# Kernel tuning notes

Measured on AMD Instinct MI355X. Metric: run time of the kernel, lower is better.

Reference implementation:

```python
import jax, jax.numpy as jnp
import numpy as np
from functools import partial

BATCH, SEQ = 2, 2048
D_MODEL, D_INNER, D_XB = 2048, 4096, 1024
HEADDIM, D_STATE = 64, 64
NHEADS = D_INNER // HEADDIM      # 64
NKV = D_XB // HEADDIM            # 16
REP = NHEADS // NKV              # 4
INTER = 8192
EPS = 1e-5
D_IN_PROJ = D_INNER + D_XB + D_XB + D_INNER + NHEADS  # z, x, B, C, dt


def setup_inputs() -> dict:
    key = jax.random.key(0)
    ks = jax.random.split(key, 8)
    g = lambda k, shape, s: (jax.random.normal(k, shape, jnp.float32) * s)
    return {
        "hidden_states": g(ks[0], (BATCH, SEQ, D_MODEL), 1.0),
        "ln_w": jnp.ones((D_MODEL,), jnp.float32),
        "ln_b": jnp.zeros((D_MODEL,), jnp.float32),
        "in_proj_w": g(ks[1], (D_IN_PROJ, D_MODEL), 0.02),
        "dt_bias": jax.random.uniform(ks[2], (NHEADS,), jnp.float32, -4.0, 0.0),
        "A_log": jnp.log(jnp.arange(1, NHEADS + 1, dtype=jnp.float32)),
        "Dp": jnp.ones((NHEADS,), jnp.float32),
        "norm_w": jnp.ones((D_INNER,), jnp.float32),
        "out_proj_w": g(ks[3], (D_MODEL, D_INNER), 0.02),
        "fc1_w": g(ks[4], (INTER, D_MODEL), 0.02),
        "fc1_b": jnp.zeros((INTER,), jnp.float32),
        "fc2_w": g(ks[5], (D_MODEL, INTER), 0.02),
        "fc2_b": jnp.zeros((D_MODEL,), jnp.float32),
    }


def _layernorm(x, w, b):
    mu = x.mean(-1, keepdims=True)
    var = ((x - mu) ** 2).mean(-1, keepdims=True)
    return (x - mu) * jax.lax.rsqrt(var + EPS) * w + b


def _ssd_scan(xh, dt, A, Bh, Ch):
    # xh: (b,l,h,p)  dt: (b,l,h)  A: (h,)  Bh,Ch: (b,l,h,n)
    dA = jnp.exp(dt * A)  # (b,l,h) discrete decay
    to_l = lambda t: jnp.moveaxis(t, 1, 0)  # time-major for scan

    def step(state, inp):
        dA_t, dt_t, x_t, B_t, C_t = inp
        state = state * dA_t[:, :, None, None] + jnp.einsum(
            "bh,bhp,bhn->bhpn", dt_t, x_t, B_t)
        y = jnp.einsum("bhpn,bhn->bhp", state, C_t)
        return state, y

    state0 = jnp.zeros((xh.shape[0], NHEADS, HEADDIM, D_STATE), xh.dtype)
    _, ys = jax.lax.scan(step, state0, (to_l(dA), to_l(dt), to_l(xh), to_l(Bh), to_l(Ch)))
    return jnp.moveaxis(ys, 0, 1)  # (b,l,h,p)


def reference(hidden_states, ln_w, ln_b, in_proj_w, dt_bias, A_log, Dp,
              norm_w, out_proj_w, fc1_w, fc1_b, fc2_w, fc2_b):
    residual = hidden_states
    h = _layernorm(hidden_states, ln_w, ln_b)

    # ---- Mamba2 branch ----
    zxbcdt = h @ in_proj_w.T  # (b,l,D_IN_PROJ)
    z, x, Bm, Cm, dt = jnp.split(
        zxbcdt, np.cumsum([D_INNER, D_XB, D_XB, D_INNER]).tolist(), axis=-1)
    b, l = h.shape[0], h.shape[1]
    dt = jax.nn.softplus(dt + dt_bias)               # (b,l,nheads)
    A = -jnp.exp(A_log)                              # (nheads,)
    # GQA-style repeat of x (values) and B (keys) from NKV to NHEADS groups
    xh = jnp.repeat(x.reshape(b, l, NKV, HEADDIM), REP, axis=2)   # (b,l,h,p)
    Bh = jnp.repeat(Bm.reshape(b, l, NKV, D_STATE), REP, axis=2)  # (b,l,h,n)
    Ch = Cm.reshape(b, l, NHEADS, D_STATE)                        # (b,l,h,n)

    y = _ssd_scan(xh, dt, A, Bh, Ch) + Dp[None, None, :, None] * xh
    yf = y.reshape(b, l, D_INNER)
    # gated RMSNorm (norm_before_gate=False): gate first, then rmsnorm
    yf = yf * jax.nn.silu(z)
    yf = yf * jax.lax.rsqrt((yf * yf).mean(-1, keepdims=True) + EPS) * norm_w
    mamba_out = yf @ out_proj_w.T

    # ---- Phi MLP branch (parallel, shares the layernormed input) ----
    mlp = jax.nn.gelu(h @ fc1_w.T + fc1_b, approximate=True) @ fc2_w.T + fc2_b

    # resid_dropout is identity in eval mode
    return mamba_out + mlp + residual
```

## Files before the change

### kernel.cpp

```cpp
#include <hip/hip_runtime.h>
#include <hip/hip_bf16.h>

#define BATCH 2
#define SEQ   2048
#define DMODEL 2048
#define DINNER 4096
#define DXB   1024
#define NHEADS 64
#define NKV   16
#define HEADDIM 64
#define DSTATE 64
#define INTER 8192
#define DINPROJ 10304
#define ROWS  (BATCH*SEQ)
#define NC    32
#define EPSV  1e-5f

typedef short short8 __attribute__((ext_vector_type(8)));
typedef float f32x4 __attribute__((ext_vector_type(4)));

typedef const __attribute__((address_space(1))) unsigned int cg_u32;
typedef __attribute__((address_space(3))) unsigned int ls_u32;

static __device__ __forceinline__ void gll16(const void* g, void* l) {
    __builtin_amdgcn_global_load_lds((cg_u32*)g, (ls_u32*)l, 16, 0, 0);
}

static __device__ __forceinline__ unsigned short f2bf(float f) {
    unsigned int u = __float_as_uint(f);
    unsigned int r = (u + 0x7fffu + ((u >> 16) & 1u)) >> 16;
    return (unsigned short)r;
}
static __device__ __forceinline__ float bf2f(unsigned short h) {
    return __uint_as_float(((unsigned int)h) << 16);
}

__global__ __launch_bounds__(256) void convk(const float* __restrict__ in,
                                             unsigned short* __restrict__ out, int n4) {
    int stride = gridDim.x * blockDim.x;
    for (int i = blockIdx.x * blockDim.x + threadIdx.x; i < n4; i += stride) {
        float4 v = ((const float4*)in)[i];
        ushort4 o;
        o.x = f2bf(v.x); o.y = f2bf(v.y); o.z = f2bf(v.z); o.w = f2bf(v.w);
        ((ushort4*)out)[i] = o;
    }
}

__global__ __launch_bounds__(256) void ln_kernel(const float* __restrict__ x,
                                                 const float* __restrict__ w,
                                                 const float* __restrict__ b,
                                                 unsigned short* __restrict__ hout) {
    int row = blockIdx.x;
    int t = threadIdx.x;
    const float* xr = x + (size_t)row * DMODEL;
    float v[8];
    float4 v0 = *(const float4*)&xr[t * 8];
    float4 v1 = *(const float4*)&xr[t * 8 + 4];
    v[0]=v0.x; v[1]=v0.y; v[2]=v0.z; v[3]=v0.w; v[4]=v1.x; v[5]=v1.y; v[6]=v1.z; v[7]=v1.w;
    float s = 0.f, s2 = 0.f;
    #pragma unroll
    for (int i = 0; i < 8; ++i) { s += v[i]; s2 += v[i]*v[i]; }
    #pragma unroll
    for (int off = 1; off < 64; off <<= 1) { s += __shfl_xor(s, off); s2 += __shfl_xor(s2, off); }
    __shared__ float sa[4], sb[4];
    int lane = t & 63, wv = t >> 6;
    if (lane == 0) { sa[wv] = s; sb[wv] = s2; }
    __syncthreads();
    s = sa[0]+sa[1]+sa[2]+sa[3];
    s2 = sb[0]+sb[1]+sb[2]+sb[3];
    float mu = s / DMODEL;
    float var = s2 / DMODEL - mu * mu;
    float sc = rsqrtf(var + EPSV);
    unsigned short* ho = hout + (size_t)row * DMODEL + t * 8;
    #pragma unroll
    for (int i = 0; i < 8; ++i) {
        int d = t * 8 + i;
        ho[i] = f2bf((v[i] - mu) * sc * w[d] + b[d]);
    }
}

#define SLOTSZ 49152
template <int EPI>
__global__ __launch_bounds__(512, 2) void gemm_p(
    const unsigned short* __restrict__ A, const unsigned short* __restrict__ B,
    int M, int N, int K, int nby,
    float* __restrict__ outF, unsigned short* __restrict__ outH,
    const float* __restrict__ bias, const float* __restrict__ add1,
    const float* __restrict__ add2) {
    __shared__ __align__(16) char smem[3 * SLOTSZ];
    int t = threadIdx.x, lane = t & 63, w = t >> 6;
    int nwg = gridDim.x, cpx = nwg >> 3;
    int logical = (blockIdx.x & 7) * cpx + (blockIdx.x >> 3);
    int by = logical % nby, bx = logical / nby;
    int brow = by * 128, bcol = bx * 256;
    int wr = w >> 2, wc = w & 3;
    int wrb = wr * 64, wcb = wc * 64;

    int lr8 = lane >> 3;
    int lch = ((lane & 7) ^ lr8) << 3;
    const unsigned short* pa[2];
    #pragma unroll
    for (int j = 0; j < 2; ++j)
        pa[j] = A + (size_t)(brow + w * 16 + j * 8 + lr8) * K + lch;
    const unsigned short* pb[4];
    #pragma unroll
    for (int j = 0; j < 4; ++j) {
        int r = bcol + w * 32 + j * 8 + lr8;
        if (r > N - 1) r = N - 1;
        pb[j] = B + (size_t)r * K + lch;
    }
    auto stageA = [&](int slot, int j) {
        gll16(pa[j], smem + slot * SLOTSZ + (w * 16 + j * 8) * 128);
        pa[j] += 64;
    };
    auto stageB = [&](int slot, int j) {
        gll16(pb[j], smem + slot * SLOTSZ + 16384 + (w * 32 + j * 8) * 128);
        pb[j] += 64;
    };

    int arow = lane & 15;
    int swz0 = (((lane >> 4) ^ (lane & 7)) << 4);

    f32x4 acc[4][4] = {};
    const int NT = K >> 6;
    #pragma unroll
    for (int j = 0; j < 2; ++j) stageA(0, j);
    #pragma unroll
    for (int j = 0; j < 4; ++j) stageB(0, j);
    #pragma unroll
    for (int j = 0; j < 2; ++j) stageA(1, j);
    #pragma unroll
    for (int j = 0; j < 4; ++j) stageB(1, j);

    int slot = 0, slot2 = 2;
    for (int kt = 0; kt < NT; ++kt) {
        if (kt + 1 < NT) { asm volatile("s_waitcnt vmcnt(6)" ::: "memory"); }
        else             { asm volatile("s_waitcnt vmcnt(0)" ::: "memory"); }
        __builtin_amdgcn_s_barrier();
        asm volatile("" ::: "memory");
        const char* Ab = smem + slot * SLOTSZ;
        const char* Bb = Ab + 16384;
        bool st = (kt + 2 < NT);
        short8 af[4], bfv[4];
        #pragma unroll
        for (int f = 0; f < 4; ++f)
            af[f] = *(const short8*)(Ab + (wrb + f * 16 + arow) * 128 + swz0);
        #pragma unroll
        for (int n = 0; n < 4; ++n)
            bfv[n] = *(const short8*)(Bb + (wcb + n * 16 + arow) * 128 + swz0);
        if (st) { stageA(slot2, 0); stageA(slot2, 1); stageB(slot2, 0); }
        __builtin_amdgcn_s_setprio(1);
        #pragma unroll
        for (int f = 0; f < 4; ++f)
            #pragma unroll
            for (int n = 0; n < 4; ++n)
                acc[f][n] = __builtin_amdgcn_mfma_f32_16x16x32_bf16(af[f], bfv[n], acc[f][n], 0, 0, 0);
        __builtin_amdgcn_s_setprio(0);
        #pragma unroll
        for (int f = 0; f < 4; ++f)
            af[f] = *(const short8*)(Ab + (wrb + f * 16 + arow) * 128 + (swz0 ^ 64));
        #pragma unroll
        for (int n = 0; n < 4; ++n)
            bfv[n] = *(const short8*)(Bb + (wcb + n * 16 + arow) * 128 + (swz0 ^ 64));
        if (st) { stageB(slot2, 1); stageB(slot2, 2); stageB(slot2, 3); }
        __builtin_amdgcn_s_setprio(1);
        #pragma unroll
        for (int f = 0; f < 4; ++f)
            #pragma unroll
            for (int n = 0; n < 4; ++n)
                acc[f][n] = __builtin_amdgcn_mfma_f32_16x16x32_bf16(af[f], bfv[n], acc[f][n], 0, 0, 0);
        __builtin_amdgcn_s_setprio(0);
        slot  = (slot  == 2) ? 0 : slot + 1;
        slot2 = (slot2 == 2) ? 0 : slot2 + 1;
    }

    int rlane = (lane >> 4) << 2, clane = lane & 15;
    #pragma unroll
    for (int f = 0; f < 4; ++f) {
        #pragma unroll
        for (int n = 0; n < 4; ++n) {
            int col = bcol + wcb + n * 16 + clane;
            if (col < N) {
                #pragma unroll
                for (int j = 0; j < 4; ++j) {
                    int row = brow + wrb + f * 16 + rlane + j;
                    size_t idx = (size_t)row * N + col;
                    float v = acc[f][n][j];
                    if constexpr (EPI == 0) {
                        outF[idx] = v;
                    } else if constexpr (EPI == 1) {
                        v += bias[col];
                        float g = 0.5f * v * (1.f + tanhf(0.7978845608f * (v + 0.044715f * v * v * v)));
                        outH[idx] = f2bf(g);
                    } else if constexpr (EPI == 2) {
                        outF[idx] = v + bias[col] + add1[idx] + add2[idx];
                    } else {
                        outH[idx] = f2bf(v);
                    }
                }
            }
        }
    }
}

__global__ __launch_bounds__(256) void dtk(const unsigned short* __restrict__ zx,
                                           const float* __restrict__ dt_bias,
                                           const float* __restrict__ A_log,
                                           float* __restrict__ dtv, float* __restrict__ dtA) {
    int idx = blockIdx.x * 256 + threadIdx.x;
    int h = idx & 63;
    size_t row = idx >> 6;
    float raw = bf2f(zx[row * DINPROJ + 10240 + h]) + dt_bias[h];
    float dt = raw > 20.f ? raw : log1pf(expf(raw));
    dtv[idx] = dt;
    dtA[idx] = dt * (-expf(A_log[h]));
}

static __device__ __forceinline__ void mm64(const unsigned short* Al, const unsigned short* Bl,
                                            f32x4* acc, int w, int lane) {
    int lr = lane & 15, kg = (lane >> 4) << 3;
    #pragma unroll
    for (int ks = 0; ks < 2; ++ks) {
        short8 a = *(const short8*)&Al[(w * 16 + lr) * 64 + ks * 32 + kg];
        #pragma unroll
        for (int fn = 0; fn < 4; ++fn) {
            short8 bb = *(const short8*)&Bl[(fn * 16 + lr) * 64 + ks * 32 + kg];
            acc[fn] = __builtin_amdgcn_mfma_f32_16x16x32_bf16(a, bb, acc[fn], 0, 0, 0);
        }
    }
}

__global__ __launch_bounds__(256) void chunk_front(const unsigned short* __restrict__ zx,
                                                   const float* __restrict__ dtv,
                                                   const float* __restrict__ dtA,
                                                   float* __restrict__ pcum,
                                                   unsigned short* __restrict__ ybuf,
                                                   unsigned short* __restrict__ Sbuf) {
    __shared__ __align__(16) unsigned short Cs[64*64], Bsr[64*64], Btr[64*64],
                                            Xtr[64*64], Xw[64*64], Wsm[64*64];
    __shared__ float dts[64], clg[64];
    int t = threadIdx.x, lane = t & 63, w = t >> 6;
    int bid = blockIdx.x;
    int c = bid & 31, h = (bid >> 5) & 63, b = bid >> 11, g = h >> 2;
    int row0 = (b << 11) + (c << 6);

    if (t < 64) {
        dts[t] = dtv[(size_t)(row0 + t) * 64 + h];
        float v = dtA[(size_t)(row0 + t) * 64 + h];
        #pragma unroll
        for (int off = 1; off < 64; off <<= 1) {
            float o = __shfl_up(v, off);
            if (lane >= off) v += o;
        }
        clg[t] = v;
        pcum[(size_t)(row0 + t) * 64 + h] = expf(v);
    }
    ushort4 xr[4];
    #pragma unroll
    for (int i = 0; i < 4; ++i) {
        int q = i * 256 + t, s = q >> 4, d4 = (q & 15) << 2;
        const unsigned short* rp = zx + (size_t)(row0 + s) * DINPROJ;
        ushort4 cv = *(const ushort4*)&rp[6144 + h * 64 + d4];
        *(ushort4*)&Cs[s * 64 + d4] = cv;
        ushort4 bv = *(const ushort4*)&rp[5120 + g * 64 + d4];
        *(ushort4*)&Bsr[s * 64 + d4] = bv;
        Btr[(d4 + 0) * 64 + s] = bv.x; Btr[(d4 + 1) * 64 + s] = bv.y;
        Btr[(d4 + 2) * 64 + s] = bv.z; Btr[(d4 + 3) * 64 + s] = bv.w;
        ushort4 xv = *(const ushort4*)&rp[4096 + g * 64 + d4];
        Xtr[(d4 + 0) * 64 + s] = xv.x; Xtr[(d4 + 1) * 64 + s] = xv.y;
        Xtr[(d4 + 2) * 64 + s] = xv.z; Xtr[(d4 + 3) * 64 + s] = xv.w;
        xr[i] = xv;
    }
    __syncthreads();
    float cl63 = clg[63];
    #pragma unroll
    for (int i = 0; i < 4; ++i) {
        int q = i * 256 + t, s = q >> 4, d4 = (q & 15) << 2;
        float ws = dts[s] * expf(cl63 - clg[s]);
        Xw[(d4 + 0) * 64 + s] = f2bf(bf2f(xr[i].x) * ws);
        Xw[(d4 + 1) * 64 + s] = f2bf(bf2f(xr[i].y) * ws);
        Xw[(d4 + 2) * 64 + s] = f2bf(bf2f(xr[i].z) * ws);
        Xw[(d4 + 3) * 64 + s] = f2bf(bf2f(xr[i].w) * ws);
    }
    __syncthreads();
    f32x4 accG[4] = {};
    mm64(Cs, Bsr, accG, w, lane);
    int rl = (lane >> 4) << 2, cl = lane & 15;
    #pragma unroll
    for (int fn = 0; fn < 4; ++fn) {
        #pragma unroll
        for (int j = 0; j < 4; ++j) {
            int tr = w * 16 + rl + j, rc = fn * 16 + cl;
            float val = 0.f;
            if (rc <= tr) val = accG[fn][j] * expf(clg[tr] - clg[rc]) * dts[rc];
            Wsm[tr * 64 + rc] = f2bf(val);
        }
    }
    __syncthreads();
    f32x4 accY[4] = {};
    mm64(Wsm, Xtr, accY, w, lane);
    f32x4 accS[4] = {};
    mm64(Xw, Btr, accS, w, lane);
    size_t cb = (size_t)((((b << 6) + h) << 5) + c) * 4096;
    #pragma unroll
    for (int fn = 0; fn < 4; ++fn) {
        #pragma unroll
        for (int j = 0; j < 4; ++j) {
            int tr = w * 16 + rl + j, pc = fn * 16 + cl;
            ybuf[(size_t)(row0 + tr) * DINNER + h * 64 + pc] = f2bf(accY[fn][j]);
            Sbuf[cb + tr * 64 + pc] = f2bf(accS[fn][j]);
        }
    }
}

__global__ __launch_bounds__(256) void chunk_state(unsigned short* __restrict__ SH,
                                                   const float* __restrict__ pcum) {
    int b = blockIdx.x >> 6, h = blockIdx.x & 63, t = threadIdx.x;
    float H[16];
    #pragma unroll
    for (int j = 0; j < 16; ++j) H[j] = 0.f;
    for (int c = 0; c < NC; ++c) {
        size_t base = (size_t)((((b << 6) + h) << 5) + c) * 4096;
        float Tc = pcum[(size_t)((b << 11) + (c << 6) + 63) * 64 + h];
        #pragma unroll
        for (int j = 0; j < 16; ++j) {
            int e = j * 256 + t;
            unsigned short sv = SH[base + e];
            SH[base + e] = f2bf(H[j]);
            H[j] = H[j] * Tc + bf2f(sv);
        }
    }
}

__global__ __launch_bounds__(256) void chunk_back(const unsigned short* __restrict__ zx,
                                                  const unsigned short* __restrict__ SH,
                                                  const float* __restrict__ pcum,
                                                  const float* __restrict__ Dp,
                                                  unsigned short* __restrict__ ybuf) {
    __shared__ __align__(16) unsigned short Cs[64*64], Hs[64*64];
    __shared__ float ps[64];
    int t = threadIdx.x, lane = t & 63, w = t >> 6;
    int bid = blockIdx.x;
    int c = bid & 31, h = (bid >> 5) & 63, b = bid >> 11, g = h >> 2;
    int row0 = (b << 11) + (c << 6);
    size_t cb = (size_t)((((b << 6) + h) << 5) + c) * 4096;
    #pragma unroll
    for (int i = 0; i < 4; ++i) {
        int q = i * 256 + t, s = q >> 4, d4 = (q & 15) << 2;
        *(ushort4*)&Cs[s * 64 + d4] =
            *(const ushort4*)&zx[(size_t)(row0 + s) * DINPROJ + 6144 + h * 64 + d4];
        *(ushort4*)&Hs[s * 64 + d4] = *(const ushort4*)&SH[cb + s * 64 + d4];
    }
    if (t < 64) ps[t] = pcum[(size_t)(row0 + t) * 64 + h];
    __syncthreads();
    f32x4 acc[4] = {};
    mm64(Cs, Hs, acc, w, lane);
    float Dph = Dp[h];
    int rl = (lane >> 4) << 2, cl = lane & 15;
    #pragma unroll
    for (int fn = 0; fn < 4; ++fn) {
        #pragma unroll
        for (int j = 0; j < 4; ++j) {
            int tr = w * 16 + rl + j, pc = fn * 16 + cl;
            size_t yi = (size_t)(row0 + tr) * DINNER + h * 64 + pc;
            float xv = bf2f(zx[(size_t)(row0 + tr) * DINPROJ + 4096 + g * 64 + pc]);
            ybuf[yi] = f2bf(bf2f(ybuf[yi]) + acc[fn][j] * ps[tr] + Dph * xv);
        }
    }
}

__global__ __launch_bounds__(256) void gate_kernel(const unsigned short* __restrict__ y,
                                                   const unsigned short* __restrict__ zx,
                                                   const float* __restrict__ norm_w,
                                                   unsigned short* __restrict__ yf) {
    int row = blockIdx.x;
    int t = threadIdx.x;
    float v[16];
    float s2 = 0.f;
    #pragma unroll
    for (int i = 0; i < 16; ++i) {
        int d = i * 256 + t;
        float yv = bf2f(y[(size_t)row * DINNER + d]);
        float zv = bf2f(zx[(size_t)row * DINPROJ + d]);
        float gt = zv / (1.f + expf(-zv));
        v[i] = yv * gt;
        s2 += v[i] * v[i];
    }
    #pragma unroll
    for (int off = 1; off < 64; off <<= 1) s2 += __shfl_xor(s2, off);
    __shared__ float sb[4];
    int lane = t & 63, wv = t >> 6;
    if (lane == 0) sb[wv] = s2;
    __syncthreads();
    s2 = sb[0] + sb[1] + sb[2] + sb[3];
    float sc = rsqrtf(s2 / DINNER + EPSV);
    #pragma unroll
    for (int i = 0; i < 16; ++i) {
        int d = i * 256 + t;
        yf[(size_t)row * DINNER + d] = f2bf(v[i] * sc * norm_w[d]);
    }
}

extern "C" void kernel_launch(void* const* d_in, const int* in_sizes, int n_in,
                              void* d_out, int out_size, void* d_ws, size_t ws_size,
                              hipStream_t stream) {
    const float* hid   = (const float*)d_in[0];
    const float* ln_w  = (const float*)d_in[1];
    const float* ln_b  = (const float*)d_in[2];
    const float* w_inp = (const float*)d_in[3];
    const float* dtb   = (const float*)d_in[4];
    const float* A_log = (const float*)d_in[5];
    const float* Dp    = (const float*)d_in[6];
    const float* nw    = (const float*)d_in[7];
    const float* w_out = (const float*)d_in[8];
    const float* w_fc1 = (const float*)d_in[9];
    const float* fc1_b = (const float*)d_in[10];
    const float* w_fc2 = (const float*)d_in[11];
    const float* fc2_b = (const float*)d_in[12];

    char* ws = (char*)d_ws;
    size_t off = 0;
    auto alloc = [&](size_t bytes) { size_t o = off; off += (bytes + 255) & ~(size_t)255; return o; };
    size_t o_h    = alloc((size_t)ROWS * DMODEL * 2);
    size_t o_w    = alloc((size_t)DINPROJ * DMODEL * 2);
    size_t o_zx   = alloc((size_t)ROWS * DINPROJ * 2);
    size_t o_dt   = alloc((size_t)ROWS * NHEADS * 4);
    size_t o_dta  = alloc((size_t)ROWS * NHEADS * 4);
    size_t o_pc   = alloc((size_t)ROWS * NHEADS * 4);
    size_t o_y    = alloc((size_t)ROWS * DINNER * 2);
    size_t o_yf   = alloc((size_t)ROWS * DINNER * 2);
    size_t o_S    = alloc((size_t)BATCH * NHEADS * NC * HEADDIM * DSTATE * 2);

    unsigned short* h_bf  = (unsigned short*)(ws + o_h);
    unsigned short* wbuf  = (unsigned short*)(ws + o_w);
    unsigned short* zx    = (unsigned short*)(ws + o_zx);
    float* dtv            = (float*)(ws + o_dt);
    float* dtA            = (float*)(ws + o_dta);
    float* pcum           = (float*)(ws + o_pc);
    unsigned short* ybuf  = (unsigned short*)(ws + o_y);
    unsigned short* yf    = (unsigned short*)(ws + o_yf);
    unsigned short* Sbuf  = (unsigned short*)(ws + o_S);
    unsigned short* gelu  = (unsigned short*)(ws + o_zx);
    float* mamba          = (float*)(ws + o_y);
    float* outF           = (float*)d_out;

    ln_kernel<<<ROWS, 256, 0, stream>>>(hid, ln_w, ln_b, h_bf);
    convk<<<2048, 256, 0, stream>>>(w_inp, wbuf, (DINPROJ * DMODEL) / 4);
    gemm_p<3><<<41 * 32, 512, 0, stream>>>(
        h_bf, wbuf, ROWS, DINPROJ, DMODEL, 32, nullptr, zx, nullptr, nullptr, nullptr);
    dtk<<<(ROWS * NHEADS) / 256, 256, 0, stream>>>(zx, dtb, A_log, dtv, dtA);
    chunk_front<<<BATCH * NHEADS * NC, 256, 0, stream>>>(zx, dtv, dtA, pcum, ybuf, Sbuf);
    chunk_state<<<BATCH * NHEADS, 256, 0, stream>>>(Sbuf, pcum);
    chunk_back<<<BATCH * NHEADS * NC, 256, 0, stream>>>(zx, Sbuf, pcum, Dp, ybuf);
    gate_kernel<<<ROWS, 256, 0, stream>>>(ybuf, zx, nw, yf);
    convk<<<2048, 256, 0, stream>>>(w_out, wbuf, (DMODEL * DINNER) / 4);
    gemm_p<0><<<8 * 32, 512, 0, stream>>>(
        yf, wbuf, ROWS, DMODEL, DINNER, 32, mamba, nullptr, nullptr, nullptr, nullptr);
    convk<<<2048, 256, 0, stream>>>(w_fc1, wbuf, (INTER * DMODEL) / 4);
    gemm_p<1><<<32 * 32, 512, 0, stream>>>(
        h_bf, wbuf, ROWS, INTER, DMODEL, 32, nullptr, gelu, fc1_b, nullptr, nullptr);
    convk<<<2048, 256, 0, stream>>>(w_fc2, wbuf, (DMODEL * INTER) / 4);
    gemm_p<2><<<8 * 32, 512, 0, stream>>>(
        gelu, wbuf, ROWS, DMODEL, INTER, 32, outF, nullptr, fc2_b, mamba, hid);
}
```

Measured before the change: 790.7 us.

## Restructure GEMM main-loop barriers and fold dt softplus into chunk_front

The bf16 GEMM main loop now has workgroup barriers between the LDS fragment reads and each MFMA block, plus an explicit lgkmcnt wait and a sched_barrier. The vmcnt wait for the next slot moves to the end of each iteration, and a prologue barrier is added before the loop. The intent is to keep waves in lockstep so loads and MFMA bursts interleave across waves, in a ping-pong style. Separately, the small dtk kernel is removed: softplus(dt + bias) and dt*A are now computed inside chunk_front, which saves a launch and two intermediate buffers. The extra barriers could add stall time if the waves do not overlap as intended.

```diff
diff --git a/kernel.cpp b/kernel.cpp
--- a/kernel.cpp
+++ b/kernel.cpp
@@ -131,13 +131,12 @@
     for (int j = 0; j < 2; ++j) stageA(1, j);
     #pragma unroll
     for (int j = 0; j < 4; ++j) stageB(1, j);
+    asm volatile("s_waitcnt vmcnt(6)" ::: "memory");
+    __builtin_amdgcn_s_barrier();
+    asm volatile("" ::: "memory");
 
     int slot = 0, slot2 = 2;
     for (int kt = 0; kt < NT; ++kt) {
-        if (kt + 1 < NT) { asm volatile("s_waitcnt vmcnt(6)" ::: "memory"); }
-        else             { asm volatile("s_waitcnt vmcnt(0)" ::: "memory"); }
-        __builtin_amdgcn_s_barrier();
-        asm volatile("" ::: "memory");
         const char* Ab = smem + slot * SLOTSZ;
         const char* Bb = Ab + 16384;
         bool st = (kt + 2 < NT);
@@ -149,6 +148,9 @@
         for (int n = 0; n < 4; ++n)
             bfv[n] = *(const short8*)(Bb + (wcb + n * 16 + arow) * 128 + swz0);
         if (st) { stageA(slot2, 0); stageA(slot2, 1); stageB(slot2, 0); }
+        __builtin_amdgcn_s_barrier();
+        asm volatile("s_waitcnt lgkmcnt(0)" ::: "memory");
+        __builtin_amdgcn_sched_barrier(0);
         __builtin_amdgcn_s_setprio(1);
         #pragma unroll
         for (int f = 0; f < 4; ++f)
@@ -156,6 +158,7 @@
             for (int n = 0; n < 4; ++n)
                 acc[f][n] = __builtin_amdgcn_mfma_f32_16x16x32_bf16(af[f], bfv[n], acc[f][n], 0, 0, 0);
         __builtin_amdgcn_s_setprio(0);
+        __builtin_amdgcn_s_barrier();
         #pragma unroll
         for (int f = 0; f < 4; ++f)
             af[f] = *(const short8*)(Ab + (wrb + f * 16 + arow) * 128 + (swz0 ^ 64));
@@ -163,6 +166,9 @@
         for (int n = 0; n < 4; ++n)
             bfv[n] = *(const short8*)(Bb + (wcb + n * 16 + arow) * 128 + (swz0 ^ 64));
         if (st) { stageB(slot2, 1); stageB(slot2, 2); stageB(slot2, 3); }
+        __builtin_amdgcn_s_barrier();
+        asm volatile("s_waitcnt lgkmcnt(0)" ::: "memory");
+        __builtin_amdgcn_sched_barrier(0);
         __builtin_amdgcn_s_setprio(1);
         #pragma unroll
         for (int f = 0; f < 4; ++f)
@@ -170,6 +176,10 @@
             for (int n = 0; n < 4; ++n)
                 acc[f][n] = __builtin_amdgcn_mfma_f32_16x16x32_bf16(af[f], bfv[n], acc[f][n], 0, 0, 0);
         __builtin_amdgcn_s_setprio(0);
+        if (kt + 2 < NT)      asm volatile("s_waitcnt vmcnt(6)" ::: "memory");
+        else if (kt + 1 < NT) asm volatile("s_waitcnt vmcnt(0)" ::: "memory");
+        __builtin_amdgcn_s_barrier();
+        asm volatile("" ::: "memory");
         slot  = (slot  == 2) ? 0 : slot + 1;
         slot2 = (slot2 == 2) ? 0 : slot2 + 1;
     }
@@ -203,19 +213,6 @@
     }
 }
 
-__global__ __launch_bounds__(256) void dtk(const unsigned short* __restrict__ zx,
-                                           const float* __restrict__ dt_bias,
-                                           const float* __restrict__ A_log,
-                                           float* __restrict__ dtv, float* __restrict__ dtA) {
-    int idx = blockIdx.x * 256 + threadIdx.x;
-    int h = idx & 63;
-    size_t row = idx >> 6;
-    float raw = bf2f(zx[row * DINPROJ + 10240 + h]) + dt_bias[h];
-    float dt = raw > 20.f ? raw : log1pf(expf(raw));
-    dtv[idx] = dt;
-    dtA[idx] = dt * (-expf(A_log[h]));
-}
-
 static __device__ __forceinline__ void mm64(const unsigned short* Al, const unsigned short* Bl,
                                             f32x4* acc, int w, int lane) {
     int lr = lane & 15, kg = (lane >> 4) << 3;
@@ -231,8 +228,8 @@
 }
 
 __global__ __launch_bounds__(256) void chunk_front(const unsigned short* __restrict__ zx,
-                                                   const float* __restrict__ dtv,
-                                                   const float* __restrict__ dtA,
+                                                   const float* __restrict__ dt_bias,
+                                                   const float* __restrict__ A_log,
                                                    float* __restrict__ pcum,
                                                    unsigned short* __restrict__ ybuf,
                                                    unsigned short* __restrict__ Sbuf) {
@@ -245,8 +242,10 @@
     int row0 = (b << 11) + (c << 6);
 
     if (t < 64) {
-        dts[t] = dtv[(size_t)(row0 + t) * 64 + h];
-        float v = dtA[(size_t)(row0 + t) * 64 + h];
+        float raw = bf2f(zx[(size_t)(row0 + t) * DINPROJ + 10240 + h]) + dt_bias[h];
+        float dt = raw > 20.f ? raw : log1pf(expf(raw));
+        dts[t] = dt;
+        float v = dt * (-expf(A_log[h]));
         #pragma unroll
         for (int off = 1; off < 64; off <<= 1) {
             float o = __shfl_up(v, off);
@@ -424,8 +423,6 @@
     size_t o_h    = alloc((size_t)ROWS * DMODEL * 2);
     size_t o_w    = alloc((size_t)DINPROJ * DMODEL * 2);
     size_t o_zx   = alloc((size_t)ROWS * DINPROJ * 2);
-    size_t o_dt   = alloc((size_t)ROWS * NHEADS * 4);
-    size_t o_dta  = alloc((size_t)ROWS * NHEADS * 4);
     size_t o_pc   = alloc((size_t)ROWS * NHEADS * 4);
     size_t o_y    = alloc((size_t)ROWS * DINNER * 2);
     size_t o_yf   = alloc((size_t)ROWS * DINNER * 2);
@@ -434,8 +431,6 @@
     unsigned short* h_bf  = (unsigned short*)(ws + o_h);
     unsigned short* wbuf  = (unsigned short*)(ws + o_w);
     unsigned short* zx    = (unsigned short*)(ws + o_zx);
-    float* dtv            = (float*)(ws + o_dt);
-    float* dtA            = (float*)(ws + o_dta);
     float* pcum           = (float*)(ws + o_pc);
     unsigned short* ybuf  = (unsigned short*)(ws + o_y);
     unsigned short* yf    = (unsigned short*)(ws + o_yf);
@@ -448,8 +443,7 @@
     convk<<<2048, 256, 0, stream>>>(w_inp, wbuf, (DINPROJ * DMODEL) / 4);
     gemm_p<3><<<41 * 32, 512, 0, stream>>>(
         h_bf, wbuf, ROWS, DINPROJ, DMODEL, 32, nullptr, zx, nullptr, nullptr, nullptr);
-    dtk<<<(ROWS * NHEADS) / 256, 256, 0, stream>>>(zx, dtb, A_log, dtv, dtA);
-    chunk_front<<<BATCH * NHEADS * NC, 256, 0, stream>>>(zx, dtv, dtA, pcum, ybuf, Sbuf);
+    chunk_front<<<BATCH * NHEADS * NC, 256, 0, stream>>>(zx, dtb, A_log, pcum, ybuf, Sbuf);
     chunk_state<<<BATCH * NHEADS, 256, 0, stream>>>(Sbuf, pcum);
     chunk_back<<<BATCH * NHEADS * NC, 256, 0, stream>>>(zx, Sbuf, pcum, Dp, ybuf);
     gate_kernel<<<ROWS, 256, 0, stream>>>(ybuf, zx, nw, yf);
```

Measured after the change: 838.8 us. +6.1%, slower.
